# Kernel optimization log

Hardware: AMD Instinct MI355X
Metric: run time of the kernel (lower is better)

## Reference

```python
import jax, jax.numpy as jnp
import numpy as np

# Config (mirrors MarketBDHConfig / BDHConfig defaults used here)
B, T = 2, 512
NUM_ASSETS, IN_FEAT = 93, 4
D = 256          # n_embd
NH = 4           # n_head
MULT = 64        # mlp_internal_dim_multiplier
NL = 6           # n_layer
NI = D * MULT // NH  # per-head internal dim N = 4096
IN_DIM = NUM_ASSETS * IN_FEAT  # 372
ROPE_THETA = 2.0 ** 16
EPS = 1e-5


def _ln(x):
    # LayerNorm over last dim, elementwise_affine=False
    m = jnp.mean(x, axis=-1, keepdims=True)
    v = jnp.mean(jnp.square(x - m), axis=-1, keepdims=True)
    return (x - m) * jax.lax.rsqrt(v + EPS)


def _rope(x, cos, sin):
    # x: [B,NH,T,NI]; cos/sin: [T, NI//2] (broadcast over B,NH)
    x1, x2 = x[..., 0::2], x[..., 1::2]
    out = jnp.stack([x1 * cos - x2 * sin, x1 * sin + x2 * cos], axis=-1)
    return out.reshape(x.shape)


def setup_inputs() -> dict:
    key = jax.random.key(0)
    ks = jax.random.split(key, 9)
    s = 0.02
    return {
        "x": jax.random.normal(ks[0], (B, T, NUM_ASSETS, IN_FEAT), jnp.float32),
        "in_W": jax.random.normal(ks[1], (IN_DIM, D), jnp.float32) * s,
        "in_b": jnp.zeros((D,), jnp.float32),
        "encoder": jax.random.normal(ks[2], (NH, D, NI), jnp.float32) * s,
        "encoder_v": jax.random.normal(ks[3], (NH, D, NI), jnp.float32) * s,
        "decoder": jax.random.normal(ks[4], (NH * NI, D), jnp.float32) * s,
        "head_W": jax.random.normal(ks[5], (D, IN_DIM), jnp.float32) * s,
        "head_b": jnp.zeros((IN_DIM,), jnp.float32),
    }


def reference(x, in_W, in_b, encoder, encoder_v, decoder, head_W, head_b):
    # input projection: [B,T,N,F] -> [B,T,IN_DIM] -> [B,T,D]
    x_flat = x.reshape(B, T, IN_DIM)
    h = _ln(x_flat @ in_W + in_b)  # [B,T,D]

    # RoPE phase tables over the internal (latent) dimension
    freqs = 1.0 / (ROPE_THETA ** (jnp.arange(0, NI, 2, dtype=jnp.float32) / NI))
    phases = jnp.arange(T, dtype=jnp.float32)[:, None] * freqs[None, :]  # [T, NI/2]
    cos, sin = jnp.cos(phases), jnp.sin(phases)

    dec = decoder.reshape(NH, NI, D)  # head-major flatten matches transpose(1,2).reshape

    for _ in range(NL):
        h_res = h
        # encode + relu-sparsify: [B,NH,T,NI]
        h_sparse = jax.nn.relu(jnp.einsum('btd,hdn->bhtn', h, encoder))
        # BDH attention: linear (no softmax), K is Q, is_causal=False -> dense scores
        qr = _rope(h_sparse, cos, sin)
        scores = jnp.einsum('bhtn,bhsn->bhts', qr, qr)  # [B,NH,T,T]
        yKV = jnp.einsum('bhts,bsd->bhtd', scores, h)    # V = h broadcast over heads
        yKV = _ln(yKV)
        y_sparse = jax.nn.relu(jnp.einsum('bhtd,hdn->bhtn', yKV, encoder_v))
        xy_sparse = h_sparse * y_sparse  # multiplicative gating (dropout p=0)
        yMLP = jnp.einsum('bhtn,hnd->btd', xy_sparse, dec)
        h = _ln(h_res + _ln(yMLP))

    pred = (h @ head_W + head_b).reshape(B, T, NUM_ASSETS, IN_FEAT)
    return pred
```

## Files before the change

### kernel.cpp

```cpp
#include <hip/hip_runtime.h>
#include <math.h>

#define B_ 2
#define T_ 512
#define D_ 256
#define NH_ 4
#define NI_ 4096
#define IN_DIM_ 372
#define NL_ 6
#define EPS_ 1e-5f

typedef unsigned short u16;
typedef __attribute__((ext_vector_type(4))) float f32x4;
typedef __attribute__((ext_vector_type(8))) short bf16x8;

__device__ __forceinline__ u16 f2b(float f) {
  union { float f; unsigned u; } v; v.f = f;
  unsigned r = v.u + 0x7fffu + ((v.u >> 16) & 1u);
  return (u16)(r >> 16);
}
__device__ __forceinline__ float b2f(u16 s) {
  union { unsigned u; float f; } v; v.u = ((unsigned)s) << 16;
  return v.f;
}

__device__ __forceinline__ void gload16(const u16* g, u16* l) {
  __builtin_amdgcn_global_load_lds(
      (const __attribute__((address_space(1))) unsigned int*)g,
      (__attribute__((address_space(3))) unsigned int*)l, 16, 0, 0);
}

#define WAITV(N) asm volatile("s_waitcnt vmcnt(" #N ")" ::: "memory")

__device__ __forceinline__ float waveSum(float v) {
  #pragma unroll
  for (int o = 32; o > 0; o >>= 1) v += __shfl_xor(v, o, 64);
  return v;
}

__device__ __forceinline__ float blkSum256(float v, float* sb4) {
  #pragma unroll
  for (int o = 32; o > 0; o >>= 1) v += __shfl_down(v, o, 64);
  int w = threadIdx.x >> 6;
  __syncthreads();
  if ((threadIdx.x & 63) == 0) sb4[w] = v;
  __syncthreads();
  return sb4[0] + sb4[1] + sb4[2] + sb4[3];
}

template <int SAMEAB>
__device__ __forceinline__ void gemm128p(const u16* __restrict__ A,
                                         const u16* __restrict__ Bt,
                                         int lda, int k0, int k1,
                                         int row0, int col0,
                                         u16* smem, f32x4 acc[4][4]) {
  const int tid = threadIdx.x;
  const int lane = tid & 63;
  const int wv = tid >> 6;
  const int wr = (wv >> 1) << 6;
  const int wc = (wv & 1) << 6;
  const int frow = lane & 15;
  const int kg = lane >> 4;
  u16* Als = smem;
  u16* Bls = smem + 12288;
  #pragma unroll
  for (int m = 0; m < 4; m++)
    #pragma unroll
    for (int n = 0; n < 4; n++) {
      f32x4 z = {0.f, 0.f, 0.f, 0.f};
      acc[m][n] = z;
    }
  auto stage = [&](int k, int buf) {
    #pragma unroll
    for (int i = 0; i < 2; i++) {
      int s = tid + (i << 8);
      int r = s >> 2;
      int c = (((s & 3) ^ (r & 3)) << 3);
      gload16(A + (long)(row0 + r) * lda + k + c, Als + buf * 4096 + s * 8);
    }
    if (!SAMEAB) {
      #pragma unroll
      for (int i = 0; i < 2; i++) {
        int s = tid + (i << 8);
        int r = s >> 2;
        int c = (((s & 3) ^ (r & 3)) << 3);
        gload16(Bt + (long)(col0 + r) * lda + k + c, Bls + buf * 4096 + s * 8);
      }
    }
  };
  const int nk = (k1 - k0) >> 5;
  stage(k0, 0);
  stage(k0 + 32, 1);
  for (int i = 0; i < nk; i++) {
    if (i + 2 < nk) {
      if (SAMEAB) WAITV(2); else WAITV(4);
      __builtin_amdgcn_s_barrier();
      stage(k0 + (i + 2) * 32, (i + 2) % 3);
    } else if (i + 1 < nk) {
      if (SAMEAB) WAITV(2); else WAITV(4);
      __builtin_amdgcn_s_barrier();
    } else {
      WAITV(0);
      __builtin_amdgcn_s_barrier();
    }
    const int bi = i % 3;
    const u16* Ab = Als + bi * 4096;
    const u16* Bb = SAMEAB ? Ab : (Bls + bi * 4096);
    bf16x8 af[4], bfv[4];
    #pragma unroll
    for (int m = 0; m < 4; m++) {
      int rr = wr + m * 16 + frow;
      af[m] = *(const bf16x8*)(Ab + rr * 32 + ((kg ^ (rr & 3)) << 3));
    }
    #pragma unroll
    for (int n = 0; n < 4; n++) {
      int rr = wc + n * 16 + frow;
      bfv[n] = *(const bf16x8*)(Bb + rr * 32 + ((kg ^ (rr & 3)) << 3));
    }
    __builtin_amdgcn_s_setprio(1);
    #pragma unroll
    for (int m = 0; m < 4; m++)
      #pragma unroll
      for (int n = 0; n < 4; n++)
        acc[m][n] = __builtin_amdgcn_mfma_f32_16x16x32_bf16(af[m], bfv[n], acc[m][n], 0, 0, 0);
    __builtin_amdgcn_s_setprio(0);
  }
  __syncthreads();
}

#define EPILOG_SETUP \
  const int lane = threadIdx.x & 63; \
  const int wv = threadIdx.x >> 6; \
  const int wr = (wv >> 1) << 6, wc = (wv & 1) << 6;

#define STAGE_FULL(EXPR) \
  _Pragma("unroll") \
  for (int m = 0; m < 4; m++) \
    _Pragma("unroll") \
    for (int n = 0; n < 4; n++) \
      _Pragma("unroll") \
      for (int r = 0; r < 4; r++) { \
        int lr = wr + m * 16 + ((lane >> 4) << 2) + r; \
        int lc = wc + n * 16 + (lane & 15); \
        float _a = acc[m][n][r]; \
        smem[lr * 128 + (lc ^ (((lr >> 2) & 7) << 3))] = f2b(EXPR); \
      } \
  __syncthreads();

__device__ __forceinline__ void storeC_full(const f32x4 acc[4][4], u16* smem,
                                            u16* Cb, int ldc, int row0, int col0,
                                            int wr, int wc, int lane) {
  const int tid = threadIdx.x;
  STAGE_FULL(_a)
  #pragma unroll
  for (int i = 0; i < 8; i++) {
    int idx = i * 256 + tid;
    int lr = idx >> 4, ch = idx & 15;
    uint4 v = *(const uint4*)(smem + lr * 128 + ((ch ^ ((lr >> 2) & 7)) << 3));
    *(uint4*)(Cb + (long)(row0 + lr) * ldc + col0 + ch * 8) = v;
  }
}

#define STAGE_HALF(EXPR) \
  if (wr == h * 64) { \
    _Pragma("unroll") \
    for (int m = 0; m < 4; m++) \
      _Pragma("unroll") \
      for (int n = 0; n < 4; n++) \
        _Pragma("unroll") \
        for (int r = 0; r < 4; r++) { \
          int lr = m * 16 + ((lane >> 4) << 2) + r; \
          int lc = wc + n * 16 + (lane & 15); \
          float _a = acc[m][n][r]; \
          smem[lr * 128 + (lc ^ (((lr >> 2) & 7) << 3))] = f2b(EXPR); \
        } \
  } \
  __syncthreads();

__device__ __forceinline__ void storeC_lds(const f32x4 acc[4][4], u16* smem,
                                           u16* Cb, int ldc, int row0, int col0,
                                           int wr, int wc, int lane) {
  const int tid = threadIdx.x;
  #pragma unroll
  for (int h = 0; h < 2; h++) {
    STAGE_HALF(_a)
    #pragma unroll
    for (int i = 0; i < 4; i++) {
      int idx = i * 256 + tid;
      int lr = idx >> 4, ch = idx & 15;
      uint4 v = *(const uint4*)(smem + lr * 128 + ((ch ^ ((lr >> 2) & 7)) << 3));
      *(uint4*)(Cb + (long)(row0 + h * 64 + lr) * ldc + col0 + ch * 8) = v;
    }
    __syncthreads();
  }
}

__global__ __launch_bounds__(256)
void k_pre(const float* __restrict__ enc, const float* __restrict__ encv,
           const float* __restrict__ dec, u16* __restrict__ enct,
           u16* __restrict__ encvt, u16* __restrict__ dect,
           unsigned* __restrict__ cs) {
  __shared__ float tile[64][65];
  int id = blockIdx.x;
  int tid = threadIdx.x;
  if (id < 4096) {
    int idx = id * 256 + tid;
    int t = idx >> 11;
    int k = idx & 2047;
    float freq = exp2f(-(float)k * (1.0f / 128.0f));
    float ph = (float)t * freq;
    cs[idx] = (unsigned)f2b(cosf(ph)) | ((unsigned)f2b(sinf(ph)) << 16);
    return;
  }
  const float* src; u16* dst; long zoff; int r0, c0, Rd, Cd;
  if (id < 6144) {
    int q = id - 4096;
    int x = q & 63, y = (q >> 6) & 3, z = q >> 8;
    src = (z < 4) ? enc : encv;
    dst = (z < 4) ? enct : encvt;
    zoff = (long)(z & 3) * D_ * NI_;
    r0 = y * 64; c0 = x * 64; Rd = D_; Cd = NI_;
  } else {
    int q = id - 6144;
    int x = q & 3, y = q >> 2;
    src = dec; dst = dect; zoff = 0;
    r0 = y * 64; c0 = x * 64; Rd = NH_ * NI_; Cd = D_;
  }
  int tr = tid >> 4, tc4 = (tid & 15) * 4;
  #pragma unroll
  for (int i = 0; i < 4; i++) {
    int r = tr + i * 16;
    f32x4 v = *(const f32x4*)(src + zoff + (long)(r0 + r) * Cd + c0 + tc4);
    tile[r][tc4 + 0] = v.x; tile[r][tc4 + 1] = v.y;
    tile[r][tc4 + 2] = v.z; tile[r][tc4 + 3] = v.w;
  }
  __syncthreads();
  #pragma unroll
  for (int i = 0; i < 4; i++) {
    int c = tr + i * 16;
    ushort4 o;
    o.x = f2b(tile[tc4 + 0][c]); o.y = f2b(tile[tc4 + 1][c]);
    o.z = f2b(tile[tc4 + 2][c]); o.w = f2b(tile[tc4 + 3][c]);
    *(ushort4*)(dst + zoff + (long)(c0 + c) * Rd + r0 + tc4) = o;
  }
}

__global__ __launch_bounds__(256)
void k_input(const float* __restrict__ x, const float* __restrict__ W,
             const float* __restrict__ b, float* __restrict__ hf,
             u16* __restrict__ hbf, u16* __restrict__ hT) {
  __shared__ float xr[2][IN_DIM_];
  __shared__ float part[4][2][D_];
  __shared__ float sb[4];
  int bt0 = blockIdx.x * 2;
  int tid = threadIdx.x;
  int wv = tid >> 6, l = tid & 63;
  for (int i = tid; i < 2 * IN_DIM_; i += 256)
    xr[i / IN_DIM_][i % IN_DIM_] = x[(long)bt0 * IN_DIM_ + i];
  __syncthreads();
  float a00 = 0, a01 = 0, a02 = 0, a03 = 0;
  float a10 = 0, a11 = 0, a12 = 0, a13 = 0;
  int kbeg = wv * 93, kend = kbeg + 93;
  for (int k = kbeg; k < kend; k++) {
    const float* Wr = W + (long)k * D_ + l;
    float w0 = Wr[0], w1 = Wr[64], w2 = Wr[128], w3 = Wr[192];
    float x0 = xr[0][k], x1 = xr[1][k];
    a00 += x0 * w0; a01 += x0 * w1; a02 += x0 * w2; a03 += x0 * w3;
    a10 += x1 * w0; a11 += x1 * w1; a12 += x1 * w2; a13 += x1 * w3;
  }
  part[wv][0][l] = a00; part[wv][0][l + 64] = a01;
  part[wv][0][l + 128] = a02; part[wv][0][l + 192] = a03;
  part[wv][1][l] = a10; part[wv][1][l + 64] = a11;
  part[wv][1][l + 128] = a12; part[wv][1][l + 192] = a13;
  __syncthreads();
  int d = tid;
  #pragma unroll
  for (int r = 0; r < 2; r++) {
    float s = part[0][r][d] + part[1][r][d] + part[2][r][d] + part[3][r][d] + b[d];
    float mean = blkSum256(s, sb) * (1.0f / D_);
    float c = s - mean;
    float var = blkSum256(c * c, sb) * (1.0f / D_);
    float out = c * rsqrtf(var + EPS_);
    int bt = bt0 + r;
    hf[(long)bt * D_ + d] = out;
    hbf[(long)bt * D_ + d] = f2b(out);
    hT[((long)(bt >> 9) * D_ + d) * T_ + (bt & 511)] = f2b(out);
  }
}

__global__ __launch_bounds__(256)
void g_enc(const u16* __restrict__ hbf, const u16* __restrict__ enct,
           const unsigned* __restrict__ cs, u16* __restrict__ qr) {
  __shared__ u16 smem[24576];
  int head = blockIdx.z;
  int row0 = blockIdx.y * 128, col0 = blockIdx.x * 128;
  f32x4 acc[4][4];
  gemm128p<0>(hbf, enct + (long)head * NI_ * D_, D_, 0, D_, row0, col0, smem, acc);
  EPILOG_SETUP
  const int tid = threadIdx.x;
  STAGE_FULL(fmaxf(_a, 0.f))
  #pragma unroll
  for (int i = 0; i < 8; i++) {
    int idx = i * 256 + tid;
    int lr = idx >> 4, ch = idx & 15;
    uint4 v = *(const uint4*)(smem + lr * 128 + ((ch ^ ((lr >> 2) & 7)) << 3));
    int gr = row0 + lr;
    int b = gr >> 9, t = gr & 511;
    int gcol = col0 + ch * 8;
    uint4 csv = *(const uint4*)(cs + (long)t * (NI_ / 2) + (gcol >> 1));
    const unsigned* pv = &v.x; const unsigned* pc = &csv.x;
    unsigned o[4];
    #pragma unroll
    for (int j = 0; j < 4; j++) {
      float v0 = b2f((u16)pv[j]), v1 = b2f((u16)(pv[j] >> 16));
      float cc = b2f((u16)pc[j]), ss = b2f((u16)(pc[j] >> 16));
      o[j] = (unsigned)f2b(v0 * cc - v1 * ss) | ((unsigned)f2b(v0 * ss + v1 * cc) << 16);
    }
    long qri = (((long)(b * NH_ + head)) * T_ + t) * NI_ + gcol;
    *(uint4*)(qr + qri) = make_uint4(o[0], o[1], o[2], o[3]);
  }
}

__global__ __launch_bounds__(256)
void g_scores(const u16* __restrict__ qr, u16* __restrict__ scpb) {
  __shared__ u16 smem[24576];
  int tix = blockIdx.x;
  int by = (tix < 4) ? 0 : (tix < 7) ? 1 : (tix < 9) ? 2 : 3;
  int sub = (by == 0) ? 0 : (by == 1) ? 3 : (by == 2) ? 5 : 6;
  int bx = tix - sub;
  int z2 = blockIdx.z;
  int z = z2 >> 2, ks = z2 & 3;
  const u16* A = qr + (long)z * T_ * NI_;
  int row0 = by * 128, col0 = bx * 128;
  f32x4 acc[4][4];
  if (by == bx)
    gemm128p<1>(A, A, NI_, ks * 1024, ks * 1024 + 1024, row0, col0, smem, acc);
  else
    gemm128p<0>(A, A, NI_, ks * 1024, ks * 1024 + 1024, row0, col0, smem, acc);
  EPILOG_SETUP
  u16* Cb = scpb + (long)(ks * 8 + z) * T_ * T_;
  storeC_full(acc, smem, Cb, T_, row0, col0, wr, wc, lane);
  if (by != bx) {
    #pragma unroll
    for (int m = 0; m < 4; m++)
      #pragma unroll
      for (int n = 0; n < 4; n++) {
        int gc = col0 + wc + n * 16 + (lane & 15);
        int gr0 = row0 + wr + m * 16 + ((lane >> 4) << 2);
        uint2 o;
        o.x = (unsigned)f2b(acc[m][n][0]) | ((unsigned)f2b(acc[m][n][1]) << 16);
        o.y = (unsigned)f2b(acc[m][n][2]) | ((unsigned)f2b(acc[m][n][3]) << 16);
        *(uint2*)(Cb + (long)gc * T_ + gr0) = o;
      }
  }
}

__global__ __launch_bounds__(256)
void g_ykv(const u16* __restrict__ scpb, const u16* __restrict__ hT,
           u16* __restrict__ ykvpb) {
  __shared__ u16 smem[16384];
  u16* Als = smem;
  u16* Bls = smem + 8192;
  int z2 = blockIdx.z;
  int z = z2 >> 2, ks = z2 & 3;
  int b = z >> 2;
  int row0 = blockIdx.y * 128, col0 = blockIdx.x * 128;
  const long SL = (long)8 * T_ * T_;
  const u16* Ab = scpb + (long)z * T_ * T_;
  const u16* Bt = hT + (long)b * D_ * T_;
  const int tid = threadIdx.x;
  const int lane = tid & 63;
  const int wv = tid >> 6;
  const int wr = (wv >> 1) << 6, wc = (wv & 1) << 6;
  const int frow = lane & 15;
  const int kg = lane >> 4;
  const int sw = frow & 7;
  f32x4 acc[4][4];
  #pragma unroll
  for (int m = 0; m < 4; m++)
    #pragma unroll
    for (int n = 0; n < 4; n++) {
      f32x4 zz = {0.f, 0.f, 0.f, 0.f};
      acc[m][n] = zz;
    }
  const int ar = tid >> 1;
  const int ac0 = (tid & 1) << 2;
  for (int k = ks * 128; k < ks * 128 + 128; k += 64) {
    long gb = (long)(row0 + ar) * T_ + k;
    #pragma unroll
    for (int j = 0; j < 4; j++) {
      int jj = ac0 + j;
      long ga = gb + (jj << 3);
      uint4 p0 = *(const uint4*)(Ab + ga);
      uint4 p1 = *(const uint4*)(Ab + SL + ga);
      uint4 p2 = *(const uint4*)(Ab + 2 * SL + ga);
      uint4 p3 = *(const uint4*)(Ab + 3 * SL + ga);
      const unsigned* q0 = &p0.x; const unsigned* q1 = &p1.x;
      const unsigned* q2 = &p2.x; const unsigned* q3 = &p3.x;
      unsigned o[4];
      #pragma unroll
      for (int w = 0; w < 4; w++) {
        float lo = b2f((u16)q0[w]) + b2f((u16)q1[w]) + b2f((u16)q2[w]) + b2f((u16)q3[w]);
        float hi = b2f((u16)(q0[w] >> 16)) + b2f((u16)(q1[w] >> 16)) +
                   b2f((u16)(q2[w] >> 16)) + b2f((u16)(q3[w] >> 16));
        o[w] = (unsigned)f2b(lo) | ((unsigned)f2b(hi) << 16);
      }
      *(uint4*)(Als + ar * 64 + ((jj ^ (ar & 7)) << 3)) = make_uint4(o[0], o[1], o[2], o[3]);
    }
    #pragma unroll
    for (int i = 0; i < 4; i++) {
      int s = tid + (i << 8);
      int r = s >> 3;
      int c = (((s & 7) ^ (r & 7)) << 3);
      gload16(Bt + (long)(col0 + r) * T_ + k + c, Bls + s * 8);
    }
    __syncthreads();
    #pragma unroll
    for (int kk = 0; kk < 2; kk++) {
      const int slot = ((((kk << 2) + kg) ^ sw) << 3);
      bf16x8 af[4], bfv[4];
      #pragma unroll
      for (int m = 0; m < 4; m++)
        af[m] = *(const bf16x8*)(Als + (wr + m * 16 + frow) * 64 + slot);
      #pragma unroll
      for (int n = 0; n < 4; n++)
        bfv[n] = *(const bf16x8*)(Bls + (wc + n * 16 + frow) * 64 + slot);
      __builtin_amdgcn_s_setprio(1);
      #pragma unroll
      for (int m = 0; m < 4; m++)
        #pragma unroll
        for (int n = 0; n < 4; n++)
          acc[m][n] = __builtin_amdgcn_mfma_f32_16x16x32_bf16(af[m], bfv[n], acc[m][n], 0, 0, 0);
      __builtin_amdgcn_s_setprio(0);
    }
    __syncthreads();
  }
  storeC_lds(acc, smem, ykvpb + (long)(ks * 8 + z) * T_ * D_, D_, row0, col0, wr, wc, lane);
}

__global__ __launch_bounds__(256)
void k_lnykv(const u16* __restrict__ ykvpb, u16* __restrict__ ykvb) {
  int row = blockIdx.x * 4 + (threadIdx.x >> 6);
  int lane = threadIdx.x & 63;
  const long SL = (long)8 * T_ * D_;
  long base = (long)row * D_ + lane * 4;
  float v0 = 0.f, v1 = 0.f, v2 = 0.f, v3 = 0.f;
  #pragma unroll
  for (int p = 0; p < 4; p++) {
    uint2 w = *(const uint2*)(ykvpb + p * SL + base);
    v0 += b2f((u16)w.x); v1 += b2f((u16)(w.x >> 16));
    v2 += b2f((u16)w.y); v3 += b2f((u16)(w.y >> 16));
  }
  float mean = waveSum(v0 + v1 + v2 + v3) * (1.0f / D_);
  float c0 = v0 - mean, c1 = v1 - mean, c2 = v2 - mean, c3 = v3 - mean;
  float var = waveSum(c0 * c0 + c1 * c1 + c2 * c2 + c3 * c3) * (1.0f / D_);
  float rs = rsqrtf(var + EPS_);
  uint2 o;
  o.x = (unsigned)f2b(c0 * rs) | ((unsigned)f2b(c1 * rs) << 16);
  o.y = (unsigned)f2b(c2 * rs) | ((unsigned)f2b(c3 * rs) << 16);
  *(uint2*)(ykvb + base) = o;
}

__global__ __launch_bounds__(256)
void g_ysp(const u16* __restrict__ ykvb, const u16* __restrict__ encvt,
           const u16* __restrict__ qr, const unsigned* __restrict__ cs,
           u16* __restrict__ xy) {
  __shared__ u16 smem[24576];
  int z = blockIdx.z;
  int b = z >> 2, head = z & 3;
  int row0 = blockIdx.y * 128, col0 = blockIdx.x * 128;
  f32x4 acc[4][4];
  gemm128p<0>(ykvb + (long)z * T_ * D_, encvt + (long)head * NI_ * D_, D_,
              0, D_, row0, col0, smem, acc);
  EPILOG_SETUP
  const int tid = threadIdx.x;
  STAGE_FULL(fmaxf(_a, 0.f))
  #pragma unroll
  for (int i = 0; i < 8; i++) {
    int idx = i * 256 + tid;
    int lr = idx >> 4, ch = idx & 15;
    uint4 v = *(const uint4*)(smem + lr * 128 + ((ch ^ ((lr >> 2) & 7)) << 3));
    int t = row0 + lr;
    int gcol = col0 + ch * 8;
    uint4 qv = *(const uint4*)(qr + ((long)z * T_ + t) * NI_ + gcol);
    uint4 csv = *(const uint4*)(cs + (long)t * (NI_ / 2) + (gcol >> 1));
    const unsigned* pv = &v.x; const unsigned* pq = &qv.x; const unsigned* pc = &csv.x;
    unsigned o[4];
    #pragma unroll
    for (int j = 0; j < 4; j++) {
      float v0 = b2f((u16)pv[j]), v1 = b2f((u16)(pv[j] >> 16));
      float q0 = b2f((u16)pq[j]), q1 = b2f((u16)(pq[j] >> 16));
      float cc = b2f((u16)pc[j]), ss = b2f((u16)(pc[j] >> 16));
      float hs0 = fmaxf(cc * q0 + ss * q1, 0.f);
      float hs1 = fmaxf(cc * q1 - ss * q0, 0.f);
      o[j] = (unsigned)f2b(hs0 * v0) | ((unsigned)f2b(hs1 * v1) << 16);
    }
    long xyi = ((long)b * T_ + t) * (NH_ * NI_) + head * NI_ + gcol;
    *(uint4*)(xy + xyi) = make_uint4(o[0], o[1], o[2], o[3]);
  }
}

__global__ __launch_bounds__(256)
void g_ymlp(const u16* __restrict__ xy, const u16* __restrict__ dect,
            u16* __restrict__ ymlppb) {
  __shared__ u16 smem[24576];
  int ks = blockIdx.z;
  int row0 = blockIdx.y * 128, col0 = blockIdx.x * 128;
  f32x4 acc[4][4];
  gemm128p<0>(xy, dect, NH_ * NI_, ks * 1024, ks * 1024 + 1024, row0, col0, smem, acc);
  EPILOG_SETUP
  storeC_full(acc, smem, ymlppb + (long)ks * (B_ * T_) * D_, D_, row0, col0, wr, wc, lane);
}

__global__ __launch_bounds__(256)
void k_dln(const u16* __restrict__ ymlppb, float* __restrict__ hf,
           u16* __restrict__ hbf, u16* __restrict__ hT) {
  int bt = blockIdx.x * 4 + (threadIdx.x >> 6);
  int lane = threadIdx.x & 63;
  const long SL = (long)(B_ * T_) * D_;
  long base = (long)bt * D_ + lane * 4;
  float v0 = 0.f, v1 = 0.f, v2 = 0.f, v3 = 0.f;
  #pragma unroll
  for (int p = 0; p < 16; p++) {
    uint2 w = *(const uint2*)(ymlppb + p * SL + base);
    v0 += b2f((u16)w.x); v1 += b2f((u16)(w.x >> 16));
    v2 += b2f((u16)w.y); v3 += b2f((u16)(w.y >> 16));
  }
  float mean = waveSum(v0 + v1 + v2 + v3) * (1.0f / D_);
  float c0 = v0 - mean, c1 = v1 - mean, c2 = v2 - mean, c3 = v3 - mean;
  float var = waveSum(c0 * c0 + c1 * c1 + c2 * c2 + c3 * c3) * (1.0f / D_);
  float rs = rsqrtf(var + EPS_);
  f32x4 hv = *(const f32x4*)(hf + base);
  float w0 = hv.x + c0 * rs, w1 = hv.y + c1 * rs;
  float w2 = hv.z + c2 * rs, w3 = hv.w + c3 * rs;
  float m2 = waveSum(w0 + w1 + w2 + w3) * (1.0f / D_);
  float e0 = w0 - m2, e1 = w1 - m2, e2 = w2 - m2, e3 = w3 - m2;
  float va2 = waveSum(e0 * e0 + e1 * e1 + e2 * e2 + e3 * e3) * (1.0f / D_);
  float rs2 = rsqrtf(va2 + EPS_);
  float o0 = e0 * rs2, o1 = e1 * rs2, o2 = e2 * rs2, o3 = e3 * rs2;
  f32x4 of = {o0, o1, o2, o3};
  *(f32x4*)(hf + base) = of;
  uint2 ob;
  ob.x = (unsigned)f2b(o0) | ((unsigned)f2b(o1) << 16);
  ob.y = (unsigned)f2b(o2) | ((unsigned)f2b(o3) << 16);
  *(uint2*)(hbf + base) = ob;
  int b = bt >> 9, t = bt & 511;
  int d0 = lane * 4;
  hT[((long)b * D_ + d0 + 0) * T_ + t] = f2b(o0);
  hT[((long)b * D_ + d0 + 1) * T_ + t] = f2b(o1);
  hT[((long)b * D_ + d0 + 2) * T_ + t] = f2b(o2);
  hT[((long)b * D_ + d0 + 3) * T_ + t] = f2b(o3);
}

__global__ __launch_bounds__(256)
void k_head(const float* __restrict__ h, const float* __restrict__ W,
            const float* __restrict__ bb, float* __restrict__ out) {
  __shared__ float hr[2][D_];
  __shared__ float part[4][2][384];
  int bt0 = blockIdx.x * 2;
  int tid = threadIdx.x;
  int wv = tid >> 6, l = tid & 63;
  for (int i = tid; i < 2 * D_; i += 256)
    hr[i >> 8][i & 255] = h[(long)bt0 * D_ + i];
  __syncthreads();
  float a0[6] = {0.f, 0.f, 0.f, 0.f, 0.f, 0.f};
  float a1[6] = {0.f, 0.f, 0.f, 0.f, 0.f, 0.f};
  int kbeg = wv * 64, kend = kbeg + 64;
  for (int k = kbeg; k < kend; k++) {
    float x0 = hr[0][k], x1 = hr[1][k];
    const float* Wr = W + (long)k * IN_DIM_;
    #pragma unroll
    for (int jj = 0; jj < 6; jj++) {
      int j = l + jj * 64;
      float w = (j < IN_DIM_) ? Wr[j] : 0.f;
      a0[jj] += x0 * w;
      a1[jj] += x1 * w;
    }
  }
  #pragma unroll
  for (int jj = 0; jj < 6; jj++) {
    int j = l + jj * 64;
    part[wv][0][j] = a0[jj];
    part[wv][1][j] = a1[jj];
  }
  __syncthreads();
  #pragma unroll
  for (int pass = 0; pass < 2; pass++) {
    int j = tid + pass * 256;
    if (j < IN_DIM_) {
      float s0 = part[0][0][j] + part[1][0][j] + part[2][0][j] + part[3][0][j] + bb[j];
      float s1 = part[0][1][j] + part[1][1][j] + part[2][1][j] + part[3][1][j] + bb[j];
      out[(long)bt0 * IN_DIM_ + j] = s0;
      out[(long)(bt0 + 1) * IN_DIM_ + j] = s1;
    }
  }
}

extern "C" void kernel_launch(void* const* d_in, const int* in_sizes, int n_in,
                              void* d_out, int out_size, void* d_ws, size_t ws_size,
                              hipStream_t stream) {
  const float* x    = (const float*)d_in[0];
  const float* in_W = (const float*)d_in[1];
  const float* in_b = (const float*)d_in[2];
  const float* enc  = (const float*)d_in[3];
  const float* encv = (const float*)d_in[4];
  const float* dec  = (const float*)d_in[5];
  const float* hW   = (const float*)d_in[6];
  const float* hb   = (const float*)d_in[7];
  float* out = (float*)d_out;

  char* p = (char*)d_ws;
  auto alloc = [&](size_t bytes) { char* r = p; p += (bytes + 255) & ~(size_t)255; return r; };
  unsigned* cs   = (unsigned*)alloc((size_t)T_ * (NI_ / 2) * 4);
  float* hf      = (float*)alloc((size_t)B_ * T_ * D_ * 4);
  u16*   hbf     = (u16*)  alloc((size_t)B_ * T_ * D_ * 2);
  u16*   hT      = (u16*)  alloc((size_t)B_ * D_ * T_ * 2);
  u16*   enct    = (u16*)  alloc((size_t)NH_ * D_ * NI_ * 2);
  u16*   encvt   = (u16*)  alloc((size_t)NH_ * D_ * NI_ * 2);
  u16*   dect    = (u16*)  alloc((size_t)NH_ * NI_ * D_ * 2);
  u16*   qr      = (u16*)  alloc((size_t)B_ * NH_ * T_ * NI_ * 2);
  u16*   xy      = (u16*)  alloc((size_t)B_ * T_ * NH_ * NI_ * 2);
  u16*   scpb    = (u16*)  alloc((size_t)4 * 8 * T_ * T_ * 2);
  u16*   ykvpb   = (u16*)  alloc((size_t)4 * 8 * T_ * D_ * 2);
  u16*   ykvb    = (u16*)  alloc((size_t)8 * T_ * D_ * 2);
  u16*   ymlppb  = (u16*)  alloc((size_t)16 * B_ * T_ * D_ * 2);

  k_pre<<<dim3(7168), dim3(256), 0, stream>>>(enc, encv, dec, enct, encvt, dect, cs);
  k_input<<<dim3(B_ * T_ / 2), dim3(256), 0, stream>>>(x, in_W, in_b, hf, hbf, hT);

  for (int l = 0; l < NL_; l++) {
    g_enc<<<dim3(32, 8, 4), dim3(256), 0, stream>>>(hbf, enct, cs, qr);
    g_scores<<<dim3(10, 1, 32), dim3(256), 0, stream>>>(qr, scpb);
    g_ykv<<<dim3(2, 4, 32), dim3(256), 0, stream>>>(scpb, hT, ykvpb);
    k_lnykv<<<dim3(1024), dim3(256), 0, stream>>>(ykvpb, ykvb);
    g_ysp<<<dim3(32, 4, 8), dim3(256), 0, stream>>>(ykvb, encvt, qr, cs, xy);
    g_ymlp<<<dim3(2, 8, 16), dim3(256), 0, stream>>>(xy, dect, ymlppb);
    k_dln<<<dim3(256), dim3(256), 0, stream>>>(ymlppb, hf, hbf, hT);
  }

  k_head<<<dim3(B_ * T_ / 2), dim3(256), 0, stream>>>(hf, hW, hb, out);
}
```

Baseline: 735.1 us.

## Fuse y_sparse encoder GEMM, gating, and decoder GEMM into one kernel

Replaces the separate g_ysp and g_ymlp kernels with a single g_fuse kernel. Each 512-thread block computes a 128x128 chunk of relu(yKV @ encoder_v), applies the RoPE/relu gating with qr in shared memory, and multiplies it directly by the decoder slice into a register accumulator. This removes the round trip of the large xy intermediate (B*T*NH*NI bf16) through global memory. In exchange the decoder reduction is split into 32 partial slices instead of 16, which doubles the partial-sum traffic read by k_dln. Decoder B fragments are loaded straight from global memory into registers, which raises register pressure.

After: 880.6 us. +19.8%, slower.

```diff
diff --git a/kernel.cpp b/kernel.cpp
--- a/kernel.cpp
+++ b/kernel.cpp
@@ -461,55 +461,164 @@
   *(uint2*)(ykvb + base) = o;
 }
 
-__global__ __launch_bounds__(256)
-void g_ysp(const u16* __restrict__ ykvb, const u16* __restrict__ encvt,
-           const u16* __restrict__ qr, const unsigned* __restrict__ cs,
-           u16* __restrict__ xy) {
+__global__ __launch_bounds__(512, 2)
+void g_fuse(const u16* __restrict__ ykvb, const u16* __restrict__ encvt,
+            const u16* __restrict__ qr, const unsigned* __restrict__ cs,
+            const u16* __restrict__ dect, u16* __restrict__ ymlppb) {
   __shared__ u16 smem[24576];
-  int z = blockIdx.z;
-  int b = z >> 2, head = z & 3;
-  int row0 = blockIdx.y * 128, col0 = blockIdx.x * 128;
-  f32x4 acc[4][4];
-  gemm128p<0>(ykvb + (long)z * T_ * D_, encvt + (long)head * NI_ * D_, D_,
-              0, D_, row0, col0, smem, acc);
-  EPILOG_SETUP
+  u16* A1 = smem;
+  u16* B1 = smem + 4096;
+  u16* S  = smem + 8192;
   const int tid = threadIdx.x;
-  STAGE_FULL(fmaxf(_a, 0.f))
-  #pragma unroll
-  for (int i = 0; i < 8; i++) {
-    int idx = i * 256 + tid;
-    int lr = idx >> 4, ch = idx & 15;
-    uint4 v = *(const uint4*)(smem + lr * 128 + ((ch ^ ((lr >> 2) & 7)) << 3));
-    int t = row0 + lr;
-    int gcol = col0 + ch * 8;
-    uint4 qv = *(const uint4*)(qr + ((long)z * T_ + t) * NI_ + gcol);
-    uint4 csv = *(const uint4*)(cs + (long)t * (NI_ / 2) + (gcol >> 1));
-    const unsigned* pv = &v.x; const unsigned* pq = &qv.x; const unsigned* pc = &csv.x;
-    unsigned o[4];
-    #pragma unroll
-    for (int j = 0; j < 4; j++) {
-      float v0 = b2f((u16)pv[j]), v1 = b2f((u16)(pv[j] >> 16));
-      float q0 = b2f((u16)pq[j]), q1 = b2f((u16)(pq[j] >> 16));
-      float cc = b2f((u16)pc[j]), ss = b2f((u16)(pc[j] >> 16));
-      float hs0 = fmaxf(cc * q0 + ss * q1, 0.f);
-      float hs1 = fmaxf(cc * q1 - ss * q0, 0.f);
-      o[j] = (unsigned)f2b(hs0 * v0) | ((unsigned)f2b(hs1 * v1) << 16);
-    }
-    long xyi = ((long)b * T_ + t) * (NH_ * NI_) + head * NI_ + gcol;
-    *(uint4*)(xy + xyi) = make_uint4(o[0], o[1], o[2], o[3]);
-  }
-}
-
-__global__ __launch_bounds__(256)
-void g_ymlp(const u16* __restrict__ xy, const u16* __restrict__ dect,
-            u16* __restrict__ ymlppb) {
-  __shared__ u16 smem[24576];
-  int ks = blockIdx.z;
-  int row0 = blockIdx.y * 128, col0 = blockIdx.x * 128;
-  f32x4 acc[4][4];
-  gemm128p<0>(xy, dect, NH_ * NI_, ks * 1024, ks * 1024 + 1024, row0, col0, smem, acc);
-  EPILOG_SETUP
-  storeC_full(acc, smem, ymlppb + (long)ks * (B_ * T_) * D_, D_, row0, col0, wr, wc, lane);
+  const int lane = tid & 63;
+  const int wv = tid >> 6;
+  const int wrq = (wv >> 2) << 6;
+  const int wcq = wv & 3;
+  const int frow = lane & 15;
+  const int kg = lane >> 4;
+  const int row0 = blockIdx.x * 128;
+  const int zks = blockIdx.y;
+  const int z = zks >> 3, ksl = zks & 7;
+  const int b = z >> 2, head = z & 3;
+  const u16* Ay = ykvb + (long)z * T_ * D_;
+  const u16* Be = encvt + (long)head * NI_ * D_;
+  const u16* Bd = dect;
+  f32x4 acc2[4][4];
+  #pragma unroll
+  for (int m = 0; m < 4; m++)
+    #pragma unroll
+    for (int n = 0; n < 4; n++) {
+      f32x4 zz = {0.f, 0.f, 0.f, 0.f};
+      acc2[m][n] = zz;
+    }
+
+  for (int ch = 0; ch < 4; ch++) {
+    const int ni0 = ksl * 512 + ch * 128;
+    bf16x8 bpre[4][4];
+    #pragma unroll
+    for (int k2 = 0; k2 < 4; k2++)
+      #pragma unroll
+      for (int n = 0; n < 4; n++) {
+        int rr = wcq * 64 + n * 16 + frow;
+        bpre[k2][n] = *(const bf16x8*)(Bd + (long)rr * (NH_ * NI_) +
+                                       head * NI_ + ni0 + k2 * 32 + kg * 8);
+      }
+    f32x4 acc1[4][2];
+    #pragma unroll
+    for (int m = 0; m < 4; m++)
+      #pragma unroll
+      for (int n = 0; n < 2; n++) {
+        f32x4 zz = {0.f, 0.f, 0.f, 0.f};
+        acc1[m][n] = zz;
+      }
+    for (int kst = 0; kst < 8; kst++) {
+      int k = kst * 32;
+      {
+        int r = tid >> 2, j = tid & 3;
+        int c = ((j ^ (r & 3)) << 3);
+        gload16(Ay + (long)(row0 + r) * D_ + k + c, A1 + tid * 8);
+        gload16(Be + (long)(ni0 + r) * D_ + k + c, B1 + tid * 8);
+      }
+      __syncthreads();
+      bf16x8 af1[4], bf1[2];
+      #pragma unroll
+      for (int m = 0; m < 4; m++) {
+        int rr = wrq + m * 16 + frow;
+        af1[m] = *(const bf16x8*)(A1 + rr * 32 + ((kg ^ (rr & 3)) << 3));
+      }
+      #pragma unroll
+      for (int n = 0; n < 2; n++) {
+        int rr = wcq * 32 + n * 16 + frow;
+        bf1[n] = *(const bf16x8*)(B1 + rr * 32 + ((kg ^ (rr & 3)) << 3));
+      }
+      __builtin_amdgcn_s_setprio(1);
+      #pragma unroll
+      for (int m = 0; m < 4; m++)
+        #pragma unroll
+        for (int n = 0; n < 2; n++)
+          acc1[m][n] = __builtin_amdgcn_mfma_f32_16x16x32_bf16(af1[m], bf1[n], acc1[m][n], 0, 0, 0);
+      __builtin_amdgcn_s_setprio(0);
+      __syncthreads();
+    }
+    #pragma unroll
+    for (int m = 0; m < 4; m++)
+      #pragma unroll
+      for (int n = 0; n < 2; n++)
+        #pragma unroll
+        for (int r = 0; r < 4; r++) {
+          int lr = wrq + m * 16 + ((lane >> 4) << 2) + r;
+          int lc = wcq * 32 + n * 16 + (lane & 15);
+          S[lr * 128 + (lc ^ ((lr & 7) << 3))] = f2b(fmaxf(acc1[m][n][r], 0.f));
+        }
+    __syncthreads();
+    #pragma unroll
+    for (int i = 0; i < 4; i++) {
+      int idx = i * 512 + tid;
+      int lr = idx >> 4, chk = idx & 15;
+      int saddr = lr * 128 + ((chk ^ (lr & 7)) << 3);
+      uint4 v = *(const uint4*)(S + saddr);
+      int t = row0 + lr;
+      int nicol = ni0 + chk * 8;
+      uint4 qv = *(const uint4*)(qr + ((long)z * T_ + t) * NI_ + nicol);
+      uint4 csv = *(const uint4*)(cs + (long)t * (NI_ / 2) + (nicol >> 1));
+      const unsigned* pv = &v.x; const unsigned* pq = &qv.x; const unsigned* pc = &csv.x;
+      unsigned o[4];
+      #pragma unroll
+      for (int j = 0; j < 4; j++) {
+        float v0 = b2f((u16)pv[j]), v1 = b2f((u16)(pv[j] >> 16));
+        float q0 = b2f((u16)pq[j]), q1 = b2f((u16)(pq[j] >> 16));
+        float cc = b2f((u16)pc[j]), ss = b2f((u16)(pc[j] >> 16));
+        float hs0 = fmaxf(cc * q0 + ss * q1, 0.f);
+        float hs1 = fmaxf(cc * q1 - ss * q0, 0.f);
+        o[j] = (unsigned)f2b(hs0 * v0) | ((unsigned)f2b(hs1 * v1) << 16);
+      }
+      *(uint4*)(S + saddr) = make_uint4(o[0], o[1], o[2], o[3]);
+    }
+    __syncthreads();
+    __builtin_amdgcn_s_setprio(1);
+    #pragma unroll
+    for (int k2 = 0; k2 < 4; k2++) {
+      bf16x8 af2[4];
+      #pragma unroll
+      for (int m = 0; m < 4; m++) {
+        int rr = wrq + m * 16 + frow;
+        af2[m] = *(const bf16x8*)(S + rr * 128 + ((k2 * 32 + kg * 8) ^ ((rr & 7) << 3)));
+      }
+      #pragma unroll
+      for (int m = 0; m < 4; m++)
+        #pragma unroll
+        for (int n = 0; n < 4; n++)
+          acc2[m][n] = __builtin_amdgcn_mfma_f32_16x16x32_bf16(af2[m], bpre[k2][n], acc2[m][n], 0, 0, 0);
+    }
+    __builtin_amdgcn_s_setprio(0);
+    __syncthreads();
+  }
+
+  u16* Cb = ymlppb + (long)(head * 8 + ksl) * (B_ * T_) * D_;
+  #pragma unroll
+  for (int dh = 0; dh < 2; dh++) {
+    if ((wcq >> 1) == dh) {
+      #pragma unroll
+      for (int m = 0; m < 4; m++)
+        #pragma unroll
+        for (int n = 0; n < 4; n++)
+          #pragma unroll
+          for (int r = 0; r < 4; r++) {
+            int lr = wrq + m * 16 + ((lane >> 4) << 2) + r;
+            int lc = (wcq & 1) * 64 + n * 16 + (lane & 15);
+            S[lr * 128 + (lc ^ ((lr & 7) << 3))] = f2b(acc2[m][n][r]);
+          }
+    }
+    __syncthreads();
+    #pragma unroll
+    for (int i = 0; i < 4; i++) {
+      int idx = i * 512 + tid;
+      int lr = idx >> 4, chh = idx & 15;
+      uint4 v = *(const uint4*)(S + lr * 128 + ((chh ^ (lr & 7)) << 3));
+      *(uint4*)(Cb + (long)(b * 512 + row0 + lr) * D_ + dh * 128 + chh * 8) = v;
+    }
+    __syncthreads();
+  }
 }
 
 __global__ __launch_bounds__(256)
@@ -521,7 +630,7 @@
   long base = (long)bt * D_ + lane * 4;
   float v0 = 0.f, v1 = 0.f, v2 = 0.f, v3 = 0.f;
   #pragma unroll
-  for (int p = 0; p < 16; p++) {
+  for (int p = 0; p < 32; p++) {
     uint2 w = *(const uint2*)(ymlppb + p * SL + base);
     v0 += b2f((u16)w.x); v1 += b2f((u16)(w.x >> 16));
     v2 += b2f((u16)w.y); v3 += b2f((u16)(w.y >> 16));
@@ -619,11 +728,10 @@
   u16*   encvt   = (u16*)  alloc((size_t)NH_ * D_ * NI_ * 2);
   u16*   dect    = (u16*)  alloc((size_t)NH_ * NI_ * D_ * 2);
   u16*   qr      = (u16*)  alloc((size_t)B_ * NH_ * T_ * NI_ * 2);
-  u16*   xy      = (u16*)  alloc((size_t)B_ * T_ * NH_ * NI_ * 2);
   u16*   scpb    = (u16*)  alloc((size_t)4 * 8 * T_ * T_ * 2);
   u16*   ykvpb   = (u16*)  alloc((size_t)4 * 8 * T_ * D_ * 2);
   u16*   ykvb    = (u16*)  alloc((size_t)8 * T_ * D_ * 2);
-  u16*   ymlppb  = (u16*)  alloc((size_t)16 * B_ * T_ * D_ * 2);
+  u16*   ymlppb  = (u16*)  alloc((size_t)32 * B_ * T_ * D_ * 2);
 
   k_pre<<<dim3(7168), dim3(256), 0, stream>>>(enc, encv, dec, enct, encvt, dect, cs);
   k_input<<<dim3(B_ * T_ / 2), dim3(256), 0, stream>>>(x, in_W, in_b, hf, hbf, hT);
@@ -633,8 +741,7 @@
     g_scores<<<dim3(10, 1, 32), dim3(256), 0, stream>>>(qr, scpb);
     g_ykv<<<dim3(2, 4, 32), dim3(256), 0, stream>>>(scpb, hT, ykvpb);
     k_lnykv<<<dim3(1024), dim3(256), 0, stream>>>(ykvpb, ykvb);
-    g_ysp<<<dim3(32, 4, 8), dim3(256), 0, stream>>>(ykvb, encvt, qr, cs, xy);
-    g_ymlp<<<dim3(2, 8, 16), dim3(256), 0, stream>>>(xy, dect, ymlppb);
+    g_fuse<<<dim3(4, 64), dim3(512), 0, stream>>>(ykvb, encvt, qr, cs, dect, ymlppb);
     k_dln<<<dim3(256), dim3(256), 0, stream>>>(ymlppb, hf, hbf, hT);
   }
 
```
